# Performance work log

Measured on AMD Instinct MI355X. Metric: run time of the kernel, lower is better.

Reference implementation:

```python
import jax, jax.numpy as jnp
import numpy as np
import math

NUM_HEADS = 2


def setup_inputs() -> dict:
    key = jax.random.key(0)
    k1, k2, k3, k4 = jax.random.split(key, 4)
    B, S, E = 16, 2048, 8  # embed_dim == n_wires == 8 (required by module structure)
    x = jax.random.normal(k1, (B, S, E), dtype=jnp.float32)
    theta = jax.random.normal(k2, (E,), dtype=jnp.float32)          # trainable RX angles, one per wire
    w_out = jax.random.normal(k3, (E, E), dtype=jnp.float32) / math.sqrt(E)  # out_proj weight
    b_out = jax.random.normal(k4, (E,), dtype=jnp.float32) * 0.01   # out_proj bias
    return {"x": x, "theta": theta, "w_out": w_out, "b_out": b_out}


def reference(x, theta, w_out, b_out):
    B, S, E = x.shape
    H = NUM_HEADS
    dk = E // H
    # Quantum projection, analytic form: per-wire RX(x) then RX(theta) on |0>,
    # PauliZ expectation -> cos(x + theta). Same layer applied for q, k, v.
    q = jnp.cos(x + theta)              # [B, S, E]
    qh = q.reshape(B, S, H, dk).transpose(0, 2, 1, 3)  # [B, H, S, dk]; q == k == v
    scores = jnp.einsum('bhqd,bhkd->bhqk', qh, qh) / jnp.sqrt(jnp.float32(dk))
    attn = jax.nn.softmax(scores, axis=-1)             # dropout is identity in eval
    out = jnp.einsum('bhqk,bhkd->bhqd', attn, qh)      # [B, H, S, dk]
    out = out.transpose(0, 2, 1, 3).reshape(B, S, E)
    return out @ w_out.T + b_out
```

## Files before the change

kernel.cpp:

```cpp
#include <hip/hip_runtime.h>
#include <math.h>

#define BB 16
#define SS 2048
#define HH 2
#define ROWS_PER_BLOCK 128
#define THREADS1 512
#define KT 16
#define NITER (SS / KT)
#define KVT_STRIDE 2064

typedef _Float16 half8 __attribute__((ext_vector_type(8)));
typedef _Float16 half4h __attribute__((ext_vector_type(4)));
typedef _Float16 half2h __attribute__((ext_vector_type(2)));
typedef float floatx4 __attribute__((ext_vector_type(4)));

__device__ __forceinline__ float fast_exp2(float x) {
  return __builtin_amdgcn_exp2f(x);
}

__device__ __forceinline__ half2h pkrtz(float a, float b) {
#if defined(__has_builtin)
#if __has_builtin(__builtin_amdgcn_cvt_pkrtz)
  return __builtin_bit_cast(half2h, __builtin_amdgcn_cvt_pkrtz(a, b));
#else
  half2h r; r[0] = (_Float16)a; r[1] = (_Float16)b; return r;
#endif
#else
  half2h r; r[0] = (_Float16)a; r[1] = (_Float16)b; return r;
#endif
}

__global__ __launch_bounds__(THREADS1, 4)
void qattn_fused(const float* __restrict__ x,
                 const float* __restrict__ theta,
                 const float* __restrict__ w_out,
                 const float* __restrict__ b_out,
                 float* __restrict__ out) {
  __shared__ half8 s_keys[SS];
  __shared__ _Float16 s_kvT[5 * KVT_STRIDE];
  __shared__ float po[ROWS_PER_BLOCK * 6];

  const int bid = blockIdx.x;
  const int rb  = bid & 15;
  const int h   = (bid >> 4) & 1;
  const int b   = bid >> 5;
  const int t   = threadIdx.x;

  const float4 th = ((const float4*)theta)[h];
  const float4* xb = (const float4*)x;

  for (int s = t; s < SS; s += THREADS1) {
    float4 xr = xb[(size_t)(b * SS + s) * 2 + h];
    _Float16 c0 = (_Float16)__cosf(xr.x + th.x);
    _Float16 c1 = (_Float16)__cosf(xr.y + th.y);
    _Float16 c2 = (_Float16)__cosf(xr.z + th.z);
    _Float16 c3 = (_Float16)__cosf(xr.w + th.w);
    const _Float16 z = (_Float16)0.0f;
    half8 v = {c0, c1, c2, c3, z, z, z, z};
    s_keys[s] = v;
    s_kvT[0 * KVT_STRIDE + s] = c0;
    s_kvT[1 * KVT_STRIDE + s] = c1;
    s_kvT[2 * KVT_STRIDE + s] = c2;
    s_kvT[3 * KVT_STRIDE + s] = c3;
  }
  for (int i = t; i < KVT_STRIDE; i += THREADS1)
    s_kvT[4 * KVT_STRIDE + i] = (_Float16)1.0f;
  __syncthreads();

  const int lane = t & 63;
  const int wv   = t >> 6;
  const int quad = lane >> 4;
  const int l15  = lane & 15;

  const float KS  = 0.72134752044448170367f;
  const float scl = (lane < 16) ? KS : 0.0f;
  const int   qrow = rb * ROWS_PER_BLOCK + wv * 16 + l15;
  half4h rq = *(const half4h*)&s_keys[qrow];
  const _Float16 z = (_Float16)0.0f;
  half8 bq = {(_Float16)((float)rq[0] * scl), (_Float16)((float)rq[1] * scl),
              (_Float16)((float)rq[2] * scl), (_Float16)((float)rq[3] * scl),
              z, z, z, z};

  const _Float16* bbase = s_kvT + (l15 < 4 ? l15 : 4) * KVT_STRIDE + quad * 4;

  floatx4 o = {0.f, 0.f, 0.f, 0.f};
  const floatx4 zf = {0.f, 0.f, 0.f, 0.f};
  half8 apv = {z, z, z, z, z, z, z, z};

#pragma unroll 4
  for (int kt = 0; kt < NITER; ++kt) {
    half8 a = s_keys[kt * KT + l15];
    half4h bl = *(const half4h*)(bbase + kt * KT);
    half8 bpv = {bl[0], bl[1], bl[2], bl[3], z, z, z, z};

    floatx4 c = __builtin_amdgcn_mfma_f32_16x16x32_f16(a, bq, zf, 0, 0, 0);

    half2h p01 = pkrtz(fast_exp2(c[0]), fast_exp2(c[1]));
    half2h p23 = pkrtz(fast_exp2(c[2]), fast_exp2(c[3]));
    apv[0] = p01[0]; apv[1] = p01[1]; apv[2] = p23[0]; apv[3] = p23[1];

    o = __builtin_amdgcn_mfma_f32_16x16x32_f16(apv, bpv, o, 0, 0, 0);
  }

  if (l15 < 5) {
#pragma unroll
    for (int r = 0; r < 4; ++r)
      po[(wv * 16 + quad * 4 + r) * 6 + l15] = o[r];
  }
  __syncthreads();

  {
    const int row = t >> 2;
    const int ep  = (t & 3) * 2;
    const float* pr = po + row * 6;
    const float inv = 1.0f / pr[4];
    const float o0 = pr[0] * inv, o1 = pr[1] * inv,
                o2 = pr[2] * inv, o3 = pr[3] * inv;
    float* op = out + ((size_t)(b * SS + rb * ROWS_PER_BLOCK + row)) * 8;
#pragma unroll
    for (int k = 0; k < 2; ++k) {
      const int e = ep + k;
      const float* wr = w_out + e * 8 + h * 4;
      float val = fmaf(o0, wr[0], fmaf(o1, wr[1], fmaf(o2, wr[2], o3 * wr[3])));
      if (h == 0) val += b_out[e];
      atomicAdd(op + e, val);
    }
  }
}

extern "C" void kernel_launch(void* const* d_in, const int* in_sizes, int n_in,
                              void* d_out, int out_size, void* d_ws, size_t ws_size,
                              hipStream_t stream) {
  const float* x     = (const float*)d_in[0];
  const float* theta = (const float*)d_in[1];
  const float* w_out = (const float*)d_in[2];
  const float* b_out = (const float*)d_in[3];
  float* out = (float*)d_out;
  (void)in_sizes; (void)n_in; (void)d_ws; (void)ws_size;

  (void)hipMemsetAsync(d_out, 0, (size_t)out_size * sizeof(float), stream);
  qattn_fused<<<dim3(BB * HH * 16), THREADS1, 0, stream>>>(x, theta, w_out, b_out, out);
}
```

Before: 80.15 us.

## Split key range across two waves per query tile and merge partials

```diff
diff --git a/kernel.cpp b/kernel.cpp
--- a/kernel.cpp
+++ b/kernel.cpp
@@ -4,10 +4,10 @@
 #define BB 16
 #define SS 2048
 #define HH 2
-#define ROWS_PER_BLOCK 128
-#define THREADS1 512
-#define KT 16
-#define NITER (SS / KT)
+#define RPB 128
+#define THREADS 1024
+#define KHALF (SS / 2)
+#define NITER (KHALF / 16)
 #define KVT_STRIDE 2064
 
 typedef _Float16 half8 __attribute__((ext_vector_type(8)));
@@ -18,20 +18,11 @@
 __device__ __forceinline__ float fast_exp2(float x) {
   return __builtin_amdgcn_exp2f(x);
 }
-
 __device__ __forceinline__ half2h pkrtz(float a, float b) {
-#if defined(__has_builtin)
-#if __has_builtin(__builtin_amdgcn_cvt_pkrtz)
   return __builtin_bit_cast(half2h, __builtin_amdgcn_cvt_pkrtz(a, b));
-#else
-  half2h r; r[0] = (_Float16)a; r[1] = (_Float16)b; return r;
-#endif
-#else
-  half2h r; r[0] = (_Float16)a; r[1] = (_Float16)b; return r;
-#endif
 }
 
-__global__ __launch_bounds__(THREADS1, 4)
+__global__ __launch_bounds__(THREADS, 8)
 void qattn_fused(const float* __restrict__ x,
                  const float* __restrict__ theta,
                  const float* __restrict__ w_out,
@@ -39,7 +30,7 @@
                  float* __restrict__ out) {
   __shared__ half8 s_keys[SS];
   __shared__ _Float16 s_kvT[5 * KVT_STRIDE];
-  __shared__ float po[ROWS_PER_BLOCK * 6];
+  __shared__ float po[RPB * 2 * 5];
 
   const int bid = blockIdx.x;
   const int rb  = bid & 15;
@@ -50,55 +41,54 @@
   const float4 th = ((const float4*)theta)[h];
   const float4* xb = (const float4*)x;
 
-  for (int s = t; s < SS; s += THREADS1) {
+  for (int s = t; s < SS; s += THREADS) {
     float4 xr = xb[(size_t)(b * SS + s) * 2 + h];
-    _Float16 c0 = (_Float16)__cosf(xr.x + th.x);
-    _Float16 c1 = (_Float16)__cosf(xr.y + th.y);
-    _Float16 c2 = (_Float16)__cosf(xr.z + th.z);
-    _Float16 c3 = (_Float16)__cosf(xr.w + th.w);
+    float c0 = __cosf(xr.x + th.x), c1 = __cosf(xr.y + th.y);
+    float c2 = __cosf(xr.z + th.z), c3 = __cosf(xr.w + th.w);
     const _Float16 z = (_Float16)0.0f;
-    half8 v = {c0, c1, c2, c3, z, z, z, z};
+    half8 v = {(_Float16)c0, (_Float16)c1, (_Float16)c2, (_Float16)c3, z, z, z, z};
     s_keys[s] = v;
-    s_kvT[0 * KVT_STRIDE + s] = c0;
-    s_kvT[1 * KVT_STRIDE + s] = c1;
-    s_kvT[2 * KVT_STRIDE + s] = c2;
-    s_kvT[3 * KVT_STRIDE + s] = c3;
+    s_kvT[0 * KVT_STRIDE + s] = (_Float16)c0;
+    s_kvT[1 * KVT_STRIDE + s] = (_Float16)c1;
+    s_kvT[2 * KVT_STRIDE + s] = (_Float16)c2;
+    s_kvT[3 * KVT_STRIDE + s] = (_Float16)c3;
   }
-  for (int i = t; i < KVT_STRIDE; i += THREADS1)
+  for (int i = t; i < KVT_STRIDE; i += THREADS)
     s_kvT[4 * KVT_STRIDE + i] = (_Float16)1.0f;
   __syncthreads();
 
   const int lane = t & 63;
   const int wv   = t >> 6;
+  const int tile = wv >> 1;
+  const int hf   = wv & 1;
   const int quad = lane >> 4;
   const int l15  = lane & 15;
 
   const float KS  = 0.72134752044448170367f;
   const float scl = (lane < 16) ? KS : 0.0f;
-  const int   qrow = rb * ROWS_PER_BLOCK + wv * 16 + l15;
-  half4h rq = *(const half4h*)&s_keys[qrow];
+  half4h rq = *(const half4h*)&s_keys[rb * RPB + tile * 16 + l15];
   const _Float16 z = (_Float16)0.0f;
   half8 bq = {(_Float16)((float)rq[0] * scl), (_Float16)((float)rq[1] * scl),
               (_Float16)((float)rq[2] * scl), (_Float16)((float)rq[3] * scl),
               z, z, z, z};
 
-  const _Float16* bbase = s_kvT + (l15 < 4 ? l15 : 4) * KVT_STRIDE + quad * 4;
+  const _Float16* bb = s_kvT + (l15 < 4 ? l15 : 4) * KVT_STRIDE + hf * KHALF + quad * 4;
+  const half8* ak = s_keys + hf * KHALF;
 
   floatx4 o = {0.f, 0.f, 0.f, 0.f};
   const floatx4 zf = {0.f, 0.f, 0.f, 0.f};
-  half8 apv = {z, z, z, z, z, z, z, z};
 
-#pragma unroll 4
+#pragma unroll 2
   for (int kt = 0; kt < NITER; ++kt) {
-    half8 a = s_keys[kt * KT + l15];
-    half4h bl = *(const half4h*)(bbase + kt * KT);
+    half8 a = ak[kt * 16 + l15];
+    half4h bl = *(const half4h*)(bb + kt * 16);
     half8 bpv = {bl[0], bl[1], bl[2], bl[3], z, z, z, z};
 
     floatx4 c = __builtin_amdgcn_mfma_f32_16x16x32_f16(a, bq, zf, 0, 0, 0);
 
     half2h p01 = pkrtz(fast_exp2(c[0]), fast_exp2(c[1]));
     half2h p23 = pkrtz(fast_exp2(c[2]), fast_exp2(c[3]));
-    apv[0] = p01[0]; apv[1] = p01[1]; apv[2] = p23[0]; apv[3] = p23[1];
+    half8 apv = {p01[0], p01[1], p23[0], p23[1], z, z, z, z};
 
     o = __builtin_amdgcn_mfma_f32_16x16x32_f16(apv, bpv, o, 0, 0, 0);
   }
@@ -106,26 +96,23 @@
   if (l15 < 5) {
 #pragma unroll
     for (int r = 0; r < 4; ++r)
-      po[(wv * 16 + quad * 4 + r) * 6 + l15] = o[r];
+      po[((tile * 16 + quad * 4 + r) * 2 + hf) * 5 + l15] = o[r];
   }
   __syncthreads();
 
   {
-    const int row = t >> 2;
-    const int ep  = (t & 3) * 2;
-    const float* pr = po + row * 6;
-    const float inv = 1.0f / pr[4];
-    const float o0 = pr[0] * inv, o1 = pr[1] * inv,
-                o2 = pr[2] * inv, o3 = pr[3] * inv;
-    float* op = out + ((size_t)(b * SS + rb * ROWS_PER_BLOCK + row)) * 8;
-#pragma unroll
-    for (int k = 0; k < 2; ++k) {
-      const int e = ep + k;
-      const float* wr = w_out + e * 8 + h * 4;
-      float val = fmaf(o0, wr[0], fmaf(o1, wr[1], fmaf(o2, wr[2], o3 * wr[3])));
-      if (h == 0) val += b_out[e];
-      atomicAdd(op + e, val);
-    }
+    const int row = t >> 3;
+    const int e   = t & 7;
+    const float* pr = po + row * 10;
+    const float n0 = pr[0] + pr[5];
+    const float n1 = pr[1] + pr[6];
+    const float n2 = pr[2] + pr[7];
+    const float n3 = pr[3] + pr[8];
+    const float inv = 1.0f / (pr[4] + pr[9]);
+    const float* wr = w_out + e * 8 + h * 4;
+    float val = fmaf(n0, wr[0], fmaf(n1, wr[1], fmaf(n2, wr[2], n3 * wr[3]))) * inv;
+    if (h == 0) val += b_out[e];
+    atomicAdd(out + ((size_t)(b * SS + rb * RPB + row)) * 8 + e, val);
   }
 }
 
@@ -140,5 +127,5 @@
   (void)in_sizes; (void)n_in; (void)d_ws; (void)ws_size;
 
   (void)hipMemsetAsync(d_out, 0, (size_t)out_size * sizeof(float), stream);
-  qattn_fused<<<dim3(BB * HH * 16), THREADS1, 0, stream>>>(x, theta, w_out, b_out, out);
+  qattn_fused<<<dim3(BB * HH * 16), THREADS, 0, stream>>>(x, theta, w_out, b_out, out);
 }
```

Result: no change. 80.54 us (+0.5%).
